# Kernel optimization log

Measured on AMD Instinct MI355X. Metric: run time of the kernel, lower is better.

Reference implementation:

```python
import jax, jax.numpy as jnp
import numpy as np
import math

B, T, C, H, S = 2, 2048, 1024, 16, 16
HD = C // H
EPS = 1e-5


def setup_inputs() -> dict:
    key = jax.random.key(0)
    ks = jax.random.split(key, 20)
    sc = 1.0 / math.sqrt(C)
    inp = {
        "x": jax.random.normal(ks[0], (B, T, C), jnp.float32),
        # A_log_fwd: log(arange(1..S)) repeated over dim (as in __init__)
        "A_log": jnp.log(jnp.tile(jnp.arange(1, S + 1, dtype=jnp.float32), (C, 1))),
        # Linear weights stored (in, out); apply as x @ W + b
        "Wd": jax.random.normal(ks[1], (C, C), jnp.float32) * sc,
        "bd": jnp.full((C,), -3.0, jnp.float32),
        "WB": jax.random.normal(ks[2], (C, S), jnp.float32) * sc,
        "WC": jax.random.normal(ks[3], (C, S), jnp.float32) * sc,
        "Wq": jax.random.normal(ks[4], (C, C), jnp.float32) * sc,
        "bq": jnp.zeros((C,), jnp.float32),
        "Wk": jax.random.normal(ks[5], (C, C), jnp.float32) * sc,
        "bk": jnp.zeros((C,), jnp.float32),
        "Wv": jax.random.normal(ks[6], (C, C), jnp.float32) * sc,
        "bv": jnp.zeros((C,), jnp.float32),
        "Wx": jax.random.normal(ks[7], (C, C), jnp.float32) * sc,
        "bx": jnp.zeros((C,), jnp.float32),
        "Wo": jax.random.normal(ks[8], (C, C), jnp.float32) * sc,
        "bo": jnp.zeros((C,), jnp.float32),
        "ln_g": jnp.ones((C,), jnp.float32),
        "ln_b": jnp.zeros((C,), jnp.float32),
        "temp": jnp.full((1, H, 1, 1), 0.5, jnp.float32),
    }
    return inp


def _forward(x, A_log, Wd, bd, WB, WC, Wq, bq, Wk, bk, Wv, bv, Wx, bx, Wo, bo, ln_g, ln_b, temp):
    x_base = x @ Wx + bx                      # (B,T,C)
    delta = jax.nn.softplus(x @ Wd + bd)      # (B,T,C)
    B_mat = x @ WB                            # (B,T,S)
    C_mat = x @ WC                            # (B,T,S)
    A = -jnp.exp(A_log)                       # (C,S)

    def scan_fn(h, inp):
        xb_t, d_t, B_t, C_t = inp             # (B,C),(B,C),(B,S),(B,S)
        bar_A = jnp.exp(d_t[..., None] * A)   # (B,C,S)
        h = bar_A * h + (d_t * xb_t)[..., None] * B_t[:, None, :]
        y = jnp.einsum('bcs,bs->bc', h, C_t)
        return h, y

    h0 = jnp.zeros((B, C, S), x.dtype)
    xs = (jnp.swapaxes(x_base, 0, 1), jnp.swapaxes(delta, 0, 1),
          jnp.swapaxes(B_mat, 0, 1), jnp.swapaxes(C_mat, 0, 1))
    _, ys = jax.lax.scan(scan_fn, h0, xs)
    out_fwd = jnp.swapaxes(ys, 0, 1)          # (B,T,C)

    # LayerNorm(x_base + out_fwd)
    hyb = x_base + out_fwd
    mu = hyb.mean(-1, keepdims=True)
    var = hyb.var(-1, keepdims=True)
    hybrid = (hyb - mu) * jax.lax.rsqrt(var + EPS) * ln_g + ln_b

    def heads(W, b):
        return (hybrid @ W + b).reshape(B, T, H, HD).transpose(0, 2, 1, 3)

    Q, K, V = heads(Wq, bq), heads(Wk, bk), heads(Wv, bv)
    scores = jnp.einsum('bhqd,bhkd->bhqk', Q, K) / math.sqrt(HD)
    scores = scores * jax.nn.softplus(temp)
    mask = jnp.tril(jnp.ones((T, T), bool))
    scores = jnp.where(mask[None, None], scores, -jnp.inf)
    attn = jax.nn.softmax(scores, axis=-1)
    out = jnp.einsum('bhqk,bhkd->bhqd', attn, V).transpose(0, 2, 1, 3).reshape(B, T, C)
    return out @ Wo + bo


def reference(x, A_log, Wd, bd, WB, WC, Wq, bq, Wk, bk, Wv, bv, Wx, bx, Wo, bo, ln_g, ln_b, temp):
    return _forward(x, A_log, Wd, bd, WB, WC, Wq, bq, Wk, bk, Wv, bv, Wx, bx, Wo, bo, ln_g, ln_b, temp)
```

## Files before the change

kernel.cpp:

```cpp
#include <hip/hip_runtime.h>
#include <math.h>

#define B_  2
#define T_  2048
#define C_  1024
#define H_  16
#define S_  16
#define HD_ 64
#define NCH 32
#define CHL 64

typedef short  short8  __attribute__((ext_vector_type(8)));
typedef unsigned short ushort8 __attribute__((ext_vector_type(8)));
typedef unsigned short ushort4v __attribute__((ext_vector_type(4)));
typedef float  f32x4   __attribute__((ext_vector_type(4)));

__device__ __forceinline__ float softplus_f(float v) {
    return fmaxf(v, 0.f) + log1pf(__expf(-fabsf(v)));
}

__device__ __forceinline__ unsigned short f2bf(float x) {
    unsigned u = __float_as_uint(x);
    u += 0x7fffu + ((u >> 16) & 1u);
    return (unsigned short)(u >> 16);
}

__device__ __forceinline__ void gload16(const unsigned short* g,
                                        unsigned short* l)
{
    __builtin_amdgcn_global_load_lds(
        (const __attribute__((address_space(1))) unsigned int*)g,
        (__attribute__((address_space(3))) unsigned int*)l, 16, 0, 0);
}

__global__ __launch_bounds__(256) void cast_bf16(const float* __restrict__ in,
                                                 unsigned short* __restrict__ out,
                                                 int n4)
{
    int i = blockIdx.x * 256 + threadIdx.x;
    if (i >= n4) return;
    float4 v = ((const float4*)in)[i];
    ushort4v o = {f2bf(v.x), f2bf(v.y), f2bf(v.z), f2bf(v.w)};
    ((ushort4v*)out)[i] = o;
}

__device__ __forceinline__ void wtrans_body(const float* __restrict__ W,
                                            unsigned short* __restrict__ WT,
                                            int bx, int by, int tid)
{
    __shared__ float t[32][33];
    const int n0 = bx * 32, k0 = by * 32;
    const int tx = tid & 31, ty = tid >> 5;
#pragma unroll
    for (int p = 0; p < 4; ++p)
        t[ty + p * 8][tx] = W[(size_t)(k0 + ty + p * 8) * C_ + n0 + tx];
    __syncthreads();
#pragma unroll
    for (int p = 0; p < 4; ++p)
        WT[(size_t)(n0 + ty + p * 8) * C_ + k0 + tx] = f2bf(t[tx][ty + p * 8]);
}

__global__ __launch_bounds__(256) void wtrans(const float* __restrict__ W,
                                              unsigned short* __restrict__ WT)
{
    wtrans_body(W, WT, blockIdx.x, blockIdx.y, threadIdx.x);
}

__global__ __launch_bounds__(256) void wtrans_multi(
    const float* __restrict__ Wx, const float* __restrict__ Wd,
    const float* __restrict__ Wq, const float* __restrict__ Wk,
    const float* __restrict__ Wv,
    unsigned short* __restrict__ Astack, unsigned short* __restrict__ Wqkv)
{
    const float* src;
    unsigned short* dst;
    switch (blockIdx.z) {
        case 0: src = Wx; dst = Astack; break;
        case 1: src = Wd; dst = Astack + (size_t)1024 * 1024; break;
        case 2: src = Wq; dst = Wqkv; break;
        case 3: src = Wk; dst = Wqkv + (size_t)1024 * 1024; break;
        default: src = Wv; dst = Wqkv + (size_t)2048 * 1024; break;
    }
    wtrans_body(src, dst, blockIdx.x, blockIdx.y, threadIdx.x);
}

__global__ __launch_bounds__(256) void prep_misc(
    const float* __restrict__ WB, const float* __restrict__ WC,
    const float* __restrict__ bx, const float* __restrict__ bd,
    const float* __restrict__ bq, const float* __restrict__ bk,
    const float* __restrict__ bv,
    unsigned short* __restrict__ Astack, float* __restrict__ biasPD,
    float* __restrict__ biasQKV)
{
    int gid = blockIdx.x * 256 + threadIdx.x;
    if (gid < 32768) {
        int w = gid >> 14, rem = gid & 16383;
        int s = rem >> 10, k = rem & 1023;
        const float* src = w ? WC : WB;
        Astack[(size_t)(2048 + w * 16 + s) * 1024 + k] = f2bf(src[k * 16 + s]);
    } else {
        int id = gid - 32768;
        if (id < 2176) {
            biasPD[id] = id < 1024 ? bx[id] : (id < 2048 ? bd[id - 1024] : 0.f);
        } else {
            int id2 = id - 2176;
            if (id2 < 3072)
                biasQKV[id2] = id2 < 1024 ? bq[id2]
                             : (id2 < 2048 ? bk[id2 - 1024] : bv[id2 - 2048]);
        }
    }
}

__global__ __launch_bounds__(256) void gemm_mfma(
    const unsigned short* __restrict__ A, const unsigned short* __restrict__ Bm,
    const float* __restrict__ bias,
    void* __restrict__ outv, void* __restrict__ out2,
    void* __restrict__ out3, void* __restrict__ out4,
    int M, int N, int K, int lda, int mode)
{
    __shared__ __align__(16) unsigned short As[4][4096];
    __shared__ __align__(16) unsigned short Bs[4][4096];

    const int tid = threadIdx.x;
    const int w = tid >> 6, lane = tid & 63;
    const int lq = lane & 15, lg = lane >> 4;
    const int wm = w >> 1, wn = w & 1;
    const int mBase = blockIdx.y * 128, nBase = blockIdx.x * 128;

    A  += (size_t)blockIdx.z * K;
    Bm += (size_t)blockIdx.z * K;

    const int c0 = tid, c1 = tid + 256;
    const int rA0 = ((c0 >> 6) << 4) + (c0 & 15), kO0 = ((c0 >> 4) & 3) << 3;
    const int rA1 = ((c1 >> 6) << 4) + (c1 & 15), kO1 = ((c1 >> 4) & 3) << 3;

    const int wL0 = w * 512;
    const int wL1 = 2048 + w * 512;

    f32x4 acc[4][4];
#pragma unroll
    for (int i = 0; i < 4; ++i)
#pragma unroll
        for (int j = 0; j < 4; ++j) acc[i][j] = (f32x4){0.f, 0.f, 0.f, 0.f};

    const unsigned short* ga0 = A  + (size_t)(mBase + rA0) * lda + kO0;
    const unsigned short* ga1 = A  + (size_t)(mBase + rA1) * lda + kO1;
    const unsigned short* gb0 = Bm + (size_t)(nBase + rA0) * lda + kO0;
    const unsigned short* gb1 = Bm + (size_t)(nBase + rA1) * lda + kO1;

    #define STAGE(bufv, k0v)                               \
        do {                                               \
            gload16(ga0 + (k0v), &As[bufv][wL0]);          \
            gload16(ga1 + (k0v), &As[bufv][wL1]);          \
            gload16(gb0 + (k0v), &Bs[bufv][wL0]);          \
            gload16(gb1 + (k0v), &Bs[bufv][wL1]);          \
        } while (0)
    #define COMPUTE(bufv)                                                       \
        do {                                                                    \
            short8 a[4], b[4];                                                  \
            _Pragma("unroll")                                                   \
            for (int i = 0; i < 4; ++i)                                         \
                a[i] = *(const short8*)&As[bufv][((wm * 4 + i) * 64 + lg * 16 + lq) * 8]; \
            _Pragma("unroll")                                                   \
            for (int j = 0; j < 4; ++j)                                         \
                b[j] = *(const short8*)&Bs[bufv][((wn * 4 + j) * 64 + lg * 16 + lq) * 8]; \
            _Pragma("unroll")                                                   \
            for (int i = 0; i < 4; ++i)                                         \
                _Pragma("unroll")                                               \
                for (int j = 0; j < 4; ++j)                                     \
                    acc[i][j] = __builtin_amdgcn_mfma_f32_16x16x32_bf16(        \
                        a[i], b[j], acc[i][j], 0, 0, 0);                        \
        } while (0)
    #define WAITV4() asm volatile("s_waitcnt vmcnt(4)" ::: "memory")
    #define WAITV0() asm volatile("s_waitcnt vmcnt(0)" ::: "memory")
    #define LGKM0()  asm volatile("s_waitcnt lgkmcnt(0)" ::: "memory")
    #define STEP(cbuf, kt)                                          \
        do {                                                        \
            if ((kt) + 32 < K) WAITV4(); else WAITV0();             \
            LGKM0();                                                \
            __builtin_amdgcn_s_barrier();                           \
            if ((kt) + 64 < K) STAGE(((cbuf) + 2) & 3, (kt) + 64);  \
            COMPUTE(cbuf);                                          \
        } while (0)

    STAGE(0, 0);
    STAGE(1, 32);

    for (int k0 = 0; k0 < K; k0 += 128) {
        STEP(0, k0);
        STEP(1, k0 + 32);
        STEP(2, k0 + 64);
        STEP(3, k0 + 96);
    }
    #undef STAGE
    #undef COMPUTE
    #undef WAITV4
    #undef WAITV0
    #undef LGKM0
    #undef STEP

    if (mode == 0) {
        float* O = blockIdx.z ? (float*)out2 : (float*)outv;
#pragma unroll
        for (int i = 0; i < 4; ++i) {
            int Rb = mBase + wm * 64 + i * 16 + lg * 4;
#pragma unroll
            for (int j = 0; j < 4; ++j) {
                int Cg = nBase + wn * 64 + j * 16 + lq;
#pragma unroll
                for (int r = 0; r < 4; ++r)
                    O[(size_t)(Rb + r) * N + Cg] = acc[i][j][r];
            }
        }
    } else if (mode == 1) {
        float* xbaseT = (float*)outv;
        float* deltaT = (float*)out2;
        float* BmT    = (float*)out3;
        float* CmT    = (float*)out4;
#pragma unroll
        for (int i = 0; i < 4; ++i) {
            int Rb = mBase + wm * 64 + i * 16 + lg * 4;
            if (Rb >= 2080) continue;
            float bb[4];
#pragma unroll
            for (int r = 0; r < 4; ++r) bb[r] = bias[Rb + r];
#pragma unroll
            for (int j = 0; j < 4; ++j) {
                int Cg = nBase + wn * 64 + j * 16 + lq;
                int b = Cg >> 11, t = Cg & (T_ - 1);
#pragma unroll
                for (int r = 0; r < 4; ++r) {
                    int R = Rb + r;
                    float v = acc[i][j][r] + bb[r];
                    if (Rb < 1024) {
                        xbaseT[((size_t)b * C_ + R) * T_ + t] = v;
                    } else if (Rb < 2048) {
                        deltaT[((size_t)b * C_ + (R - 1024)) * T_ + t] =
                            softplus_f(v);
                    } else if (Rb < 2064) {
                        BmT[((size_t)b * S_ + (R - 2048)) * T_ + t] = v;
                    } else {
                        CmT[((size_t)b * S_ + (R - 2064)) * T_ + t] = v;
                    }
                }
            }
        }
    } else {
        unsigned short* Qb  = (unsigned short*)outv;
        unsigned short* Kb  = (unsigned short*)out2;
        unsigned short* VTb = (unsigned short*)out3;
#pragma unroll
        for (int j = 0; j < 4; ++j) {
            int Cg = nBase + wn * 64 + j * 16 + lq;
            int reg = Cg >> 10, c = Cg & 1023;
            int h = c >> 6, hd = c & 63;
            float bb = bias[Cg];
#pragma unroll
            for (int i = 0; i < 4; ++i) {
                int Rb = mBase + wm * 64 + i * 16 + lg * 4;
#pragma unroll
                for (int r = 0; r < 4; ++r) {
                    int R = Rb + r, b = R >> 11, t = R & (T_ - 1);
                    unsigned short o = f2bf(acc[i][j][r] + bb);
                    if (reg == 0)
                        Qb[(((size_t)(b * H_ + h) * T_ + t) * HD_) + hd] = o;
                    else if (reg == 1)
                        Kb[(((size_t)(b * H_ + h) * T_ + t) * HD_) + hd] = o;
                    else
                        VTb[(((size_t)(b * H_ + h) * HD_ + hd) * T_) + t] = o;
                }
            }
        }
    }
}

__global__ __launch_bounds__(256) void combine_out(
    const float* __restrict__ p0, const float* __restrict__ p1,
    const float* __restrict__ bo, float* __restrict__ out)
{
    int i = blockIdx.x * 256 + threadIdx.x;
    float4 a = ((const float4*)p0)[i];
    float4 b = ((const float4*)p1)[i];
    float4 bb = ((const float4*)bo)[i & 255];
    float4 o = {a.x + b.x + bb.x, a.y + b.y + bb.y,
                a.z + b.z + bb.z, a.w + b.w + bb.w};
    ((float4*)out)[i] = o;
}

__global__ __launch_bounds__(256) void scan_partial(
    const float* __restrict__ xbaseT, const float* __restrict__ deltaT,
    const float* __restrict__ BmT, const float* __restrict__ A_log,
    float4* __restrict__ Pbuf, float4* __restrict__ Lbuf)
{
    const int tid = threadIdx.x;
    const int s4 = tid & 3;
    const int cm = tid >> 2;
    const int cg = blockIdx.x & 15;
    const int k  = (blockIdx.x >> 4) & (NCH - 1);
    const int b  = blockIdx.x >> 9;
    const int c  = cg * 64 + cm;

    float a[4];
#pragma unroll
    for (int j = 0; j < 4; ++j)
        a[j] = -__expf(A_log[c * S_ + s4 * 4 + j]);

    const int tb = k * CHL;
    const float* dp = deltaT + ((size_t)b * C_ + c) * T_ + tb;
    const float* xp = xbaseT + ((size_t)b * C_ + c) * T_ + tb;
    const float* bp = BmT + ((size_t)(b * S_ + s4 * 4)) * T_ + tb;

    float L[4] = {0.f, 0.f, 0.f, 0.f};
    float sumd = 0.f;
    for (int t0 = 0; t0 < CHL; t0 += 4) {
        float4 d4 = *(const float4*)&dp[t0];
        float4 x4 = *(const float4*)&xp[t0];
        float dv[4] = {d4.x, d4.y, d4.z, d4.w};
        float xv[4] = {x4.x, x4.y, x4.z, x4.w};
        float bv[4][4];
#pragma unroll
        for (int j = 0; j < 4; ++j) {
            float4 b4 = *(const float4*)&bp[(size_t)j * T_ + t0];
            bv[j][0] = b4.x; bv[j][1] = b4.y; bv[j][2] = b4.z; bv[j][3] = b4.w;
        }
#pragma unroll
        for (int q = 0; q < 4; ++q) {
            float u = dv[q] * xv[q];
            sumd += dv[q];
#pragma unroll
            for (int j = 0; j < 4; ++j)
                L[j] = fmaf(__expf(dv[q] * a[j]), L[j], u * bv[j][q]);
        }
    }
    int gid = blockIdx.x * 256 + tid;
    float4 P4 = {__expf(a[0] * sumd), __expf(a[1] * sumd),
                 __expf(a[2] * sumd), __expf(a[3] * sumd)};
    float4 L4 = {L[0], L[1], L[2], L[3]};
    Pbuf[gid] = P4;
    Lbuf[gid] = L4;
}

__global__ __launch_bounds__(256) void scan_final(
    const float* __restrict__ xbaseT, const float* __restrict__ deltaT,
    const float* __restrict__ BmT, const float* __restrict__ CmT,
    const float* __restrict__ A_log, const float4* __restrict__ Pbuf,
    const float4* __restrict__ Lbuf, float* __restrict__ hyb)
{
    const int tid = threadIdx.x;
    const int s4 = tid & 3;
    const int cm = tid >> 2;
    const int cg = blockIdx.x & 15;
    const int k  = (blockIdx.x >> 4) & (NCH - 1);
    const int b  = blockIdx.x >> 9;
    const int c  = cg * 64 + cm;

    float h[4] = {0.f, 0.f, 0.f, 0.f};
    for (int k2 = 0; k2 < k; ++k2) {
        int gid2 = (((b * NCH + k2) << 4) + cg) * 256 + tid;
        float4 P4 = Pbuf[gid2];
        float4 L4 = Lbuf[gid2];
        h[0] = fmaf(P4.x, h[0], L4.x);
        h[1] = fmaf(P4.y, h[1], L4.y);
        h[2] = fmaf(P4.z, h[2], L4.z);
        h[3] = fmaf(P4.w, h[3], L4.w);
    }

    float a[4];
#pragma unroll
    for (int j = 0; j < 4; ++j)
        a[j] = -__expf(A_log[c * S_ + s4 * 4 + j]);

    const int tb = k * CHL;
    const float* dp = deltaT + ((size_t)b * C_ + c) * T_ + tb;
    const float* xp = xbaseT + ((size_t)b * C_ + c) * T_ + tb;
    const float* bp = BmT + ((size_t)(b * S_ + s4 * 4)) * T_ + tb;
    const float* cp = CmT + ((size_t)(b * S_ + s4 * 4)) * T_ + tb;
    float* hp = hyb + ((size_t)b * T_ + tb) * C_ + c;

    for (int t0 = 0; t0 < CHL; t0 += 4) {
        float4 d4 = *(const float4*)&dp[t0];
        float4 x4 = *(const float4*)&xp[t0];
        float dv[4] = {d4.x, d4.y, d4.z, d4.w};
        float xv[4] = {x4.x, x4.y, x4.z, x4.w};
        float bv[4][4], cv[4][4];
#pragma unroll
        for (int j = 0; j < 4; ++j) {
            float4 b4 = *(const float4*)&bp[(size_t)j * T_ + t0];
            float4 c4 = *(const float4*)&cp[(size_t)j * T_ + t0];
            bv[j][0] = b4.x; bv[j][1] = b4.y; bv[j][2] = b4.z; bv[j][3] = b4.w;
            cv[j][0] = c4.x; cv[j][1] = c4.y; cv[j][2] = c4.z; cv[j][3] = c4.w;
        }
#pragma unroll
        for (int q = 0; q < 4; ++q) {
            float u = dv[q] * xv[q];
#pragma unroll
            for (int j = 0; j < 4; ++j)
                h[j] = fmaf(__expf(dv[q] * a[j]), h[j], u * bv[j][q]);
            float y = h[0] * cv[0][q];
            y = fmaf(h[1], cv[1][q], y);
            y = fmaf(h[2], cv[2][q], y);
            y = fmaf(h[3], cv[3][q], y);
            y += __shfl_xor(y, 1, 64);
            y += __shfl_xor(y, 2, 64);
            if (s4 == 0) hp[(size_t)(t0 + q) * C_] = xv[q] + y;
        }
    }
}

__global__ __launch_bounds__(256) void layernorm_kernel(
    const float* __restrict__ in, const float* __restrict__ g,
    const float* __restrict__ beta, unsigned short* __restrict__ out)
{
    const int row = blockIdx.x;
    const float* rp = in + (size_t)row * C_;
    const int c = threadIdx.x * 4;
    float4 v = *(const float4*)&rp[c];
    float sum = v.x + v.y + v.z + v.w;
    float sq = v.x * v.x + v.y * v.y + v.z * v.z + v.w * v.w;
#pragma unroll
    for (int off = 1; off < 64; off <<= 1) {
        sum += __shfl_xor(sum, off, 64);
        sq += __shfl_xor(sq, off, 64);
    }
    __shared__ float sS[4], sQ[4];
    int wave = threadIdx.x >> 6, lane = threadIdx.x & 63;
    if (lane == 0) { sS[wave] = sum; sQ[wave] = sq; }
    __syncthreads();
    sum = sS[0] + sS[1] + sS[2] + sS[3];
    sq = sQ[0] + sQ[1] + sQ[2] + sQ[3];
    const float mu = sum * (1.f / C_);
    const float var = sq * (1.f / C_) - mu * mu;
    const float rstd = rsqrtf(var + 1e-5f);
    float4 gg = *(const float4*)&g[c];
    float4 bb = *(const float4*)&beta[c];
    ushort4v o;
    o.x = f2bf((v.x - mu) * rstd * gg.x + bb.x);
    o.y = f2bf((v.y - mu) * rstd * gg.y + bb.y);
    o.z = f2bf((v.z - mu) * rstd * gg.z + bb.z);
    o.w = f2bf((v.w - mu) * rstd * gg.w + bb.w);
    *(ushort4v*)&out[(size_t)row * C_ + c] = o;
}

#define BKT 128
#define KP  72
#define VP  136
__global__ __launch_bounds__(256) void attn_mfma(
    const unsigned short* __restrict__ Q, const unsigned short* __restrict__ K,
    const unsigned short* __restrict__ VT, const float* __restrict__ temp,
    unsigned short* __restrict__ out)
{
    __shared__ __align__(16) unsigned short Ks[BKT * KP];
    __shared__ __align__(16) unsigned short Vs[80 * VP];
    __shared__ __align__(16) unsigned short Ps[64 * VP];

    const int tid = threadIdx.x;
    const int w = tid >> 6, lane = tid & 63;
    const int lq = lane & 15, lg = lane >> 4;
    const int p  = blockIdx.x & 15;
    const int bh = blockIdx.x >> 4;
    const int b = bh >> 4, h = bh & 15;

    const float scale = softplus_f(temp[h]) * 0.125f;
    const unsigned short* Qp = Q + (size_t)bh * T_ * HD_;
    const unsigned short* Kp = K + (size_t)bh * T_ * HD_;
    const unsigned short* Vp = VT + (size_t)bh * HD_ * T_;

    {
        int r = 64 + (tid >> 4), o = (tid & 15) * 8;
        ushort8 ones = {0x3f80, 0x3f80, 0x3f80, 0x3f80,
                        0x3f80, 0x3f80, 0x3f80, 0x3f80};
        *(ushort8*)&Vs[r * VP + o] = ones;
    }

    ushort8 kreg[4], vreg[4];
    #define LOADKV(jtv)                                                        \
        do {                                                                   \
            int kb = (jtv) * BKT;                                              \
            _Pragma("unroll")                                                  \
            for (int q2 = 0; q2 < 4; ++q2) {                                   \
                int c = tid + q2 * 256;                                        \
                kreg[q2] = *(const ushort8*)&Kp[(size_t)(kb + (c >> 3)) * HD_  \
                                                + (c & 7) * 8];                \
                vreg[q2] = *(const ushort8*)&Vp[(size_t)(c >> 4) * T_ + kb     \
                                                + (c & 15) * 8];               \
            }                                                                  \
        } while (0)

    for (int half = 0; half < 2; ++half) {
        const int qi = half ? p : (31 - p);
        const int qbase = qi * 64;
        const int nT = (qbase + 64 + BKT - 1) / BKT;

        short8 qf[2];
#pragma unroll
        for (int s = 0; s < 2; ++s)
            qf[s] = *(const short8*)&Qp[(size_t)(qbase + w * 16 + lq) * HD_
                                        + s * 32 + lg * 8];
        LOADKV(0);

        float m_i[4];
        f32x4 o[5];
#pragma unroll
        for (int r = 0; r < 4; ++r) m_i[r] = -INFINITY;
#pragma unroll
        for (int j = 0; j < 5; ++j) o[j] = (f32x4){0.f, 0.f, 0.f, 0.f};

        for (int jt = 0; jt < nT; ++jt) {
            const int kbase = jt * BKT;
            const bool last = (jt == nT - 1);
            __syncthreads();
#pragma unroll
            for (int q2 = 0; q2 < 4; ++q2) {
                int c = tid + q2 * 256;
                *(ushort8*)&Ks[(c >> 3) * KP + (c & 7) * 8] = kreg[q2];
                *(ushort8*)&Vs[(c >> 4) * VP + (c & 15) * 8] = vreg[q2];
            }
            __syncthreads();
            if (jt + 1 < nT) LOADKV(jt + 1);

            f32x4 sacc[8];
#pragma unroll
            for (int j = 0; j < 8; ++j) sacc[j] = (f32x4){0.f, 0.f, 0.f, 0.f};
#pragma unroll
            for (int s = 0; s < 2; ++s) {
#pragma unroll
                for (int j = 0; j < 8; ++j) {
                    short8 kf = *(const short8*)&Ks[(j * 16 + lq) * KP
                                                    + s * 32 + lg * 8];
                    sacc[j] = __builtin_amdgcn_mfma_f32_16x16x32_bf16(
                        qf[s], kf, sacc[j], 0, 0, 0);
                }
            }

#pragma unroll
            for (int r = 0; r < 4; ++r) {
                int qrow = qbase + w * 16 + lg * 4 + r;
                float sv[8];
#pragma unroll
                for (int j = 0; j < 8; ++j) {
                    sv[j] = sacc[j][r] * scale;
                    if (last && (kbase + j * 16 + lq > qrow)) sv[j] = -INFINITY;
                }
                float mx = sv[0];
#pragma unroll
                for (int j = 1; j < 8; ++j) mx = fmaxf(mx, sv[j]);
                mx = fmaxf(mx, __shfl_xor(mx, 1, 64));
                mx = fmaxf(mx, __shfl_xor(mx, 2, 64));
                mx = fmaxf(mx, __shfl_xor(mx, 4, 64));
                mx = fmaxf(mx, __shfl_xor(mx, 8, 64));
                float mnew = fmaxf(m_i[r], mx);
                float alpha = __expf(m_i[r] - mnew);
                m_i[r] = mnew;
#pragma unroll
                for (int j = 0; j < 5; ++j) o[j][r] *= alpha;
#pragma unroll
                for (int j = 0; j < 8; ++j)
                    Ps[(w * 16 + lg * 4 + r) * VP + j * 16 + lq] =
                        f2bf(__expf(sv[j] - mnew));
            }

#pragma unroll
            for (int s2 = 0; s2 < 4; ++s2) {
                short8 pf = *(const short8*)&Ps[(w * 16 + lq) * VP
                                                + s2 * 32 + lg * 8];
#pragma unroll
                for (int j = 0; j < 5; ++j) {
                    short8 vf = *(const short8*)&Vs[(j * 16 + lq) * VP
                                                    + s2 * 32 + lg * 8];
                    o[j] = __builtin_amdgcn_mfma_f32_16x16x32_bf16(
                        pf, vf, o[j], 0, 0, 0);
                }
            }
        }

#pragma unroll
        for (int r = 0; r < 4; ++r) {
            float inv = 1.f / o[4][r];
            int qrow = qbase + w * 16 + lg * 4 + r;
#pragma unroll
            for (int j = 0; j < 4; ++j)
                out[((size_t)(b * T_ + qrow)) * C_ + h * 64 + j * 16 + lq] =
                    f2bf(o[j][r] * inv);
        }
    }
    #undef LOADKV
}

extern "C" void kernel_launch(void* const* d_in, const int* in_sizes, int n_in,
                              void* d_out, int out_size, void* d_ws, size_t ws_size,
                              hipStream_t stream)
{
    const float* x     = (const float*)d_in[0];
    const float* A_log = (const float*)d_in[1];
    const float* Wd    = (const float*)d_in[2];
    const float* bd    = (const float*)d_in[3];
    const float* WB    = (const float*)d_in[4];
    const float* WC    = (const float*)d_in[5];
    const float* Wq    = (const float*)d_in[6];
    const float* bq    = (const float*)d_in[7];
    const float* Wk    = (const float*)d_in[8];
    const float* bk    = (const float*)d_in[9];
    const float* Wv    = (const float*)d_in[10];
    const float* bv    = (const float*)d_in[11];
    const float* Wx    = (const float*)d_in[12];
    const float* bx    = (const float*)d_in[13];
    const float* Wo    = (const float*)d_in[14];
    const float* bo    = (const float*)d_in[15];
    const float* ln_g  = (const float*)d_in[16];
    const float* ln_b  = (const float*)d_in[17];
    const float* temp  = (const float*)d_in[18];

    char* wsb = (char*)d_ws;
    const size_t MB = 1024 * 1024;
    const size_t HMB = 512 * 1024;
    unsigned short* xb      = (unsigned short*)(wsb);
    float4* Pbuf            = (float4*)(wsb);
    float4* Lbuf            = (float4*)(wsb + 4 * MB);
    unsigned short* hybrid  = (unsigned short*)(wsb);
    float* P1               = (float*)(wsb);
    unsigned short* Astack  = (unsigned short*)(wsb + 8 * MB);
    float* biasPD           = (float*)(wsb + 8 * MB + (size_t)2176 * 2048);
    float* biasQKV          = biasPD + 2176;
    unsigned short* WqkvT   = (unsigned short*)(wsb + 12 * MB + HMB);
    unsigned short* WoT     = (unsigned short*)(wsb + 18 * MB + HMB);
    float* deltaT           = (float*)(wsb + 18 * MB + HMB);
    float* xbaseT           = (float*)(wsb + 34 * MB + HMB);
    float* hyb              = (float*)(wsb + 50 * MB + HMB);
    float* BmT              = (float*)(wsb + 66 * MB + HMB);
    float* CmT              = BmT + (size_t)B_ * S_ * T_;
    unsigned short* Qb      = (unsigned short*)(wsb + 20 * MB + HMB);
    unsigned short* Kb      = (unsigned short*)(wsb + 28 * MB + HMB);
    unsigned short* VTb     = (unsigned short*)(wsb + 36 * MB + HMB);
    unsigned short* attnO   = (unsigned short*)(wsb + 44 * MB + HMB);
    float* P0               = (float*)(wsb + 20 * MB + HMB);

    cast_bf16<<<4096, 256, 0, stream>>>(x, xb, (B_ * T_ * C_) / 4);
    wtrans_multi<<<dim3(32, 32, 5), 256, 0, stream>>>(Wx, Wd, Wq, Wk, Wv,
                                                      Astack, WqkvT);
    prep_misc<<<149, 256, 0, stream>>>(WB, WC, bx, bd, bq, bk, bv,
                                       Astack, biasPD, biasQKV);

    gemm_mfma<<<dim3(32, 17, 1), 256, 0, stream>>>(
        Astack, xb, biasPD, xbaseT, deltaT, BmT, CmT,
        2176, 4096, 1024, 1024, 1);

    const int scanBlocks = B_ * NCH * (C_ / 64);
    scan_partial<<<scanBlocks, 256, 0, stream>>>(xbaseT, deltaT, BmT, A_log,
                                                 Pbuf, Lbuf);
    scan_final<<<scanBlocks, 256, 0, stream>>>(xbaseT, deltaT, BmT, CmT, A_log,
                                               Pbuf, Lbuf, hyb);

    layernorm_kernel<<<B_ * T_, 256, 0, stream>>>(hyb, ln_g, ln_b, hybrid);

    gemm_mfma<<<dim3(24, 32, 1), 256, 0, stream>>>(
        hybrid, WqkvT, biasQKV, Qb, Kb, VTb, nullptr,
        4096, 3072, 1024, 1024, 2);

    attn_mfma<<<B_ * H_ * 16, 256, 0, stream>>>(Qb, Kb, VTb, temp, attnO);

    wtrans<<<dim3(32, 32), 256, 0, stream>>>(Wo, WoT);
    gemm_mfma<<<dim3(8, 32, 2), 256, 0, stream>>>(
        attnO, WoT, nullptr, P0, P1, nullptr, nullptr,
        4096, 1024, 512, 1024, 0);
    combine_out<<<4096, 256, 0, stream>>>(P0, P1, bo, (float*)d_out);
}
```

Measured before the change: 474.0 us.

## Use 256x256-tile 512-thread MFMA GEMM for the input and QKV projections

Adds a new GEMM kernel with 256x256 output tiles, 8 waves and double-buffered 64-wide K stages in LDS, and uses it for the fused input projection and the QKV projection. The old 128-tile kernel is kept only for the output projection and is reduced to its plain-store epilogue. Larger tiles give more data reuse per LDS load and fewer global reads. In exchange the grids shrink to 144 and 192 blocks, fewer than the CUs on the device. The 128KB LDS footprint allows only one block per CU, and the 2176-row projection now reads A rows past the end of the matrix.

```diff
diff --git a/kernel.cpp b/kernel.cpp
--- a/kernel.cpp
+++ b/kernel.cpp
@@ -111,12 +111,154 @@
     }
 }
 
-__global__ __launch_bounds__(256) void gemm_mfma(
+__global__ __launch_bounds__(512, 2) void gemm_mfma(
     const unsigned short* __restrict__ A, const unsigned short* __restrict__ Bm,
     const float* __restrict__ bias,
     void* __restrict__ outv, void* __restrict__ out2,
     void* __restrict__ out3, void* __restrict__ out4,
     int M, int N, int K, int lda, int mode)
+{
+    __shared__ __align__(16) unsigned short As[2][16384];
+    __shared__ __align__(16) unsigned short Bs[2][16384];
+
+    const int tid = threadIdx.x;
+    const int w = tid >> 6, lane = tid & 63;
+    const int lq = lane & 15, lg = lane >> 4;
+    const int wm = w >> 2, wn = w & 3;
+    const int mBase = blockIdx.y * 256, nBase = blockIdx.x * 256;
+
+    const unsigned short* gA[4];
+    const unsigned short* gB[4];
+    int ldsOff[4];
+#pragma unroll
+    for (int q = 0; q < 4; ++q) {
+        int c = tid + q * 512;
+        int row = ((c >> 7) << 4) + (c & 15);
+        int kofs = ((c >> 4) & 7) << 3;
+        gA[q] = A  + (size_t)(mBase + row) * lda + kofs;
+        gB[q] = Bm + (size_t)(nBase + row) * lda + kofs;
+        ldsOff[q] = c * 8;
+    }
+
+    f32x4 acc[8][4];
+#pragma unroll
+    for (int i = 0; i < 8; ++i)
+#pragma unroll
+        for (int j = 0; j < 4; ++j) acc[i][j] = (f32x4){0.f, 0.f, 0.f, 0.f};
+
+    #define STAGE(bufv, kt)                                   \
+        do {                                                  \
+            _Pragma("unroll")                                 \
+            for (int q = 0; q < 4; ++q) {                     \
+                gload16(gA[q] + (kt), &As[bufv][ldsOff[q]]);  \
+                gload16(gB[q] + (kt), &Bs[bufv][ldsOff[q]]);  \
+            }                                                 \
+        } while (0)
+    #define COMPUTE(bufv)                                                        \
+        do {                                                                     \
+            _Pragma("unroll")                                                    \
+            for (int s = 0; s < 2; ++s) {                                        \
+                short8 a[8], b[4];                                               \
+                _Pragma("unroll")                                                \
+                for (int i = 0; i < 8; ++i)                                      \
+                    a[i] = *(const short8*)&As[bufv][(wm * 8 + i) * 1024         \
+                                                     + (s * 4 + lg) * 128        \
+                                                     + lq * 8];                  \
+                _Pragma("unroll")                                                \
+                for (int j = 0; j < 4; ++j)                                      \
+                    b[j] = *(const short8*)&Bs[bufv][(wn * 4 + j) * 1024         \
+                                                     + (s * 4 + lg) * 128        \
+                                                     + lq * 8];                  \
+                _Pragma("unroll")                                                \
+                for (int i = 0; i < 8; ++i)                                      \
+                    _Pragma("unroll")                                            \
+                    for (int j = 0; j < 4; ++j)                                  \
+                        acc[i][j] = __builtin_amdgcn_mfma_f32_16x16x32_bf16(     \
+                            a[i], b[j], acc[i][j], 0, 0, 0);                     \
+            }                                                                    \
+        } while (0)
+
+    STAGE(0, 0);
+    __syncthreads();
+    const int nt = K >> 6;
+    for (int t = 0; t < nt; t += 2) {
+        if (t + 1 < nt) STAGE(1, (t + 1) << 6);
+        COMPUTE(0);
+        __syncthreads();
+        if (t + 2 < nt) STAGE(0, (t + 2) << 6);
+        COMPUTE(1);
+        __syncthreads();
+    }
+    #undef STAGE
+    #undef COMPUTE
+
+    if (mode == 1) {
+        float* xbaseT = (float*)outv;
+        float* deltaT = (float*)out2;
+        float* BmT    = (float*)out3;
+        float* CmT    = (float*)out4;
+#pragma unroll
+        for (int i = 0; i < 8; ++i) {
+            int Rb = mBase + wm * 128 + i * 16 + lg * 4;
+            if (Rb >= 2080) continue;
+            float bb[4];
+#pragma unroll
+            for (int r = 0; r < 4; ++r) bb[r] = bias[Rb + r];
+#pragma unroll
+            for (int j = 0; j < 4; ++j) {
+                int Cg = nBase + wn * 64 + j * 16 + lq;
+                int b = Cg >> 11, t = Cg & (T_ - 1);
+#pragma unroll
+                for (int r = 0; r < 4; ++r) {
+                    int R = Rb + r;
+                    float v = acc[i][j][r] + bb[r];
+                    if (Rb < 1024) {
+                        xbaseT[((size_t)b * C_ + R) * T_ + t] = v;
+                    } else if (Rb < 2048) {
+                        deltaT[((size_t)b * C_ + (R - 1024)) * T_ + t] =
+                            softplus_f(v);
+                    } else if (Rb < 2064) {
+                        BmT[((size_t)b * S_ + (R - 2048)) * T_ + t] = v;
+                    } else {
+                        CmT[((size_t)b * S_ + (R - 2064)) * T_ + t] = v;
+                    }
+                }
+            }
+        }
+    } else {
+        unsigned short* Qb  = (unsigned short*)outv;
+        unsigned short* Kb  = (unsigned short*)out2;
+        unsigned short* VTb = (unsigned short*)out3;
+#pragma unroll
+        for (int j = 0; j < 4; ++j) {
+            int Cg = nBase + wn * 64 + j * 16 + lq;
+            int reg = Cg >> 10, c = Cg & 1023;
+            int h = c >> 6, hd = c & 63;
+            float bb = bias[Cg];
+#pragma unroll
+            for (int i = 0; i < 8; ++i) {
+                int Rb = mBase + wm * 128 + i * 16 + lg * 4;
+#pragma unroll
+                for (int r = 0; r < 4; ++r) {
+                    int R = Rb + r, b = R >> 11, t = R & (T_ - 1);
+                    unsigned short o = f2bf(acc[i][j][r] + bb);
+                    if (reg == 0)
+                        Qb[(((size_t)(b * H_ + h) * T_ + t) * HD_) + hd] = o;
+                    else if (reg == 1)
+                        Kb[(((size_t)(b * H_ + h) * T_ + t) * HD_) + hd] = o;
+                    else
+                        VTb[(((size_t)(b * H_ + h) * HD_ + hd) * T_) + t] = o;
+                }
+            }
+        }
+    }
+}
+
+__global__ __launch_bounds__(256) void gemm_mfma128(
+    const unsigned short* __restrict__ A, const unsigned short* __restrict__ Bm,
+    const float* __restrict__ bias,
+    void* __restrict__ outv, void* __restrict__ out2,
+    int M, int N, int K, int lda)
 {
     __shared__ __align__(16) unsigned short As[4][4096];
     __shared__ __align__(16) unsigned short Bs[4][4096];
@@ -199,77 +341,16 @@
     #undef LGKM0
     #undef STEP
 
-    if (mode == 0) {
-        float* O = blockIdx.z ? (float*)out2 : (float*)outv;
-#pragma unroll
-        for (int i = 0; i < 4; ++i) {
-            int Rb = mBase + wm * 64 + i * 16 + lg * 4;
-#pragma unroll
-            for (int j = 0; j < 4; ++j) {
-                int Cg = nBase + wn * 64 + j * 16 + lq;
-#pragma unroll
-                for (int r = 0; r < 4; ++r)
-                    O[(size_t)(Rb + r) * N + Cg] = acc[i][j][r];
-            }
-        }
-    } else if (mode == 1) {
-        float* xbaseT = (float*)outv;
-        float* deltaT = (float*)out2;
-        float* BmT    = (float*)out3;
-        float* CmT    = (float*)out4;
-#pragma unroll
-        for (int i = 0; i < 4; ++i) {
-            int Rb = mBase + wm * 64 + i * 16 + lg * 4;
-            if (Rb >= 2080) continue;
-            float bb[4];
-#pragma unroll
-            for (int r = 0; r < 4; ++r) bb[r] = bias[Rb + r];
-#pragma unroll
-            for (int j = 0; j < 4; ++j) {
-                int Cg = nBase + wn * 64 + j * 16 + lq;
-                int b = Cg >> 11, t = Cg & (T_ - 1);
-#pragma unroll
-                for (int r = 0; r < 4; ++r) {
-                    int R = Rb + r;
-                    float v = acc[i][j][r] + bb[r];
-                    if (Rb < 1024) {
-                        xbaseT[((size_t)b * C_ + R) * T_ + t] = v;
-                    } else if (Rb < 2048) {
-                        deltaT[((size_t)b * C_ + (R - 1024)) * T_ + t] =
-                            softplus_f(v);
-                    } else if (Rb < 2064) {
-                        BmT[((size_t)b * S_ + (R - 2048)) * T_ + t] = v;
-                    } else {
-                        CmT[((size_t)b * S_ + (R - 2064)) * T_ + t] = v;
-                    }
-                }
-            }
-        }
-    } else {
-        unsigned short* Qb  = (unsigned short*)outv;
-        unsigned short* Kb  = (unsigned short*)out2;
-        unsigned short* VTb = (unsigned short*)out3;
+    float* O = blockIdx.z ? (float*)out2 : (float*)outv;
+#pragma unroll
+    for (int i = 0; i < 4; ++i) {
+        int Rb = mBase + wm * 64 + i * 16 + lg * 4;
 #pragma unroll
         for (int j = 0; j < 4; ++j) {
             int Cg = nBase + wn * 64 + j * 16 + lq;
-            int reg = Cg >> 10, c = Cg & 1023;
-            int h = c >> 6, hd = c & 63;
-            float bb = bias[Cg];
-#pragma unroll
-            for (int i = 0; i < 4; ++i) {
-                int Rb = mBase + wm * 64 + i * 16 + lg * 4;
-#pragma unroll
-                for (int r = 0; r < 4; ++r) {
-                    int R = Rb + r, b = R >> 11, t = R & (T_ - 1);
-                    unsigned short o = f2bf(acc[i][j][r] + bb);
-                    if (reg == 0)
-                        Qb[(((size_t)(b * H_ + h) * T_ + t) * HD_) + hd] = o;
-                    else if (reg == 1)
-                        Kb[(((size_t)(b * H_ + h) * T_ + t) * HD_) + hd] = o;
-                    else
-                        VTb[(((size_t)(b * H_ + h) * HD_ + hd) * T_) + t] = o;
-                }
-            }
+#pragma unroll
+            for (int r = 0; r < 4; ++r)
+                O[(size_t)(Rb + r) * N + Cg] = acc[i][j][r];
         }
     }
 }
@@ -640,7 +721,7 @@
     prep_misc<<<149, 256, 0, stream>>>(WB, WC, bx, bd, bq, bk, bv,
                                        Astack, biasPD, biasQKV);
 
-    gemm_mfma<<<dim3(32, 17, 1), 256, 0, stream>>>(
+    gemm_mfma<<<dim3(16, 9, 1), 512, 0, stream>>>(
         Astack, xb, biasPD, xbaseT, deltaT, BmT, CmT,
         2176, 4096, 1024, 1024, 1);
 
@@ -652,15 +733,15 @@
 
     layernorm_kernel<<<B_ * T_, 256, 0, stream>>>(hyb, ln_g, ln_b, hybrid);
 
-    gemm_mfma<<<dim3(24, 32, 1), 256, 0, stream>>>(
+    gemm_mfma<<<dim3(12, 16, 1), 512, 0, stream>>>(
         hybrid, WqkvT, biasQKV, Qb, Kb, VTb, nullptr,
         4096, 3072, 1024, 1024, 2);
 
     attn_mfma<<<B_ * H_ * 16, 256, 0, stream>>>(Qb, Kb, VTb, temp, attnO);
 
     wtrans<<<dim3(32, 32), 256, 0, stream>>>(Wo, WoT);
-    gemm_mfma<<<dim3(8, 32, 2), 256, 0, stream>>>(
-        attnO, WoT, nullptr, P0, P1, nullptr, nullptr,
-        4096, 1024, 512, 1024, 0);
+    gemm_mfma128<<<dim3(8, 32, 2), 256, 0, stream>>>(
+        attnO, WoT, nullptr, P0, P1,
+        4096, 1024, 512, 1024);
     combine_out<<<4096, 256, 0, stream>>>(P0, P1, bo, (float*)d_out);
 }
```

Measured after the change: 527.8 us. 11.3% more time.

## Add 256x256-tile 512-thread MFMA GEMM for input and QKV projections

Applied to the files above, without the earlier changes.

Introduces a new GEMM kernel that uses 256x256 output tiles with 8 waves, double-buffered LDS split into K halves, and interleaved global prefetch with barrier-gated phases and s_setprio around the MFMA bursts. The input projection and QKV projection launch this kernel, while the output projection keeps the 128x128 kernel, now specialised to the plain store mode. Larger tiles raise arithmetic intensity and cut global loads per FLOP. In exchange the grids become small (144 and 192 blocks) relative to the CU count, and register pressure rises to 32 accumulators per lane. The M=2176 input-projection GEMM is padded to 2304 rows, which wastes some work.

```diff
diff --git a/kernel.cpp b/kernel.cpp
--- a/kernel.cpp
+++ b/kernel.cpp
@@ -111,12 +111,175 @@
     }
 }
 
-__global__ __launch_bounds__(256) void gemm_mfma(
+__global__ __launch_bounds__(512, 2) void gemm_mfma256(
     const unsigned short* __restrict__ A, const unsigned short* __restrict__ Bm,
     const float* __restrict__ bias,
     void* __restrict__ outv, void* __restrict__ out2,
     void* __restrict__ out3, void* __restrict__ out4,
     int M, int N, int K, int lda, int mode)
+{
+    __shared__ __align__(16) unsigned short AS[2][2][8192];
+    __shared__ __align__(16) unsigned short BS[2][2][8192];
+
+    const int tid = threadIdx.x;
+    const int w = tid >> 6, lane = tid & 63;
+    const int lq = lane & 15, lg = lane >> 4;
+    const int wm = w >> 2, wn = w & 3;
+    const int mBase = blockIdx.y * 256, nBase = blockIdx.x * 256;
+
+    const int c0 = tid, c1 = tid + 512;
+    const int r0 = ((c0 >> 6) << 4) | (c0 & 15), k0l = ((c0 >> 4) & 3) << 3;
+    const int r1 = ((c1 >> 6) << 4) | (c1 & 15), k1l = ((c1 >> 4) & 3) << 3;
+    const unsigned short* gA0 = A  + (size_t)(mBase + r0) * lda + k0l;
+    const unsigned short* gA1 = A  + (size_t)(mBase + r1) * lda + k1l;
+    const unsigned short* gB0 = Bm + (size_t)(nBase + r0) * lda + k0l;
+    const unsigned short* gB1 = Bm + (size_t)(nBase + r1) * lda + k1l;
+
+    f32x4 acc[8][4];
+#pragma unroll
+    for (int i = 0; i < 8; ++i)
+#pragma unroll
+        for (int j = 0; j < 4; ++j) acc[i][j] = (f32x4){0.f, 0.f, 0.f, 0.f};
+
+    #define STG_A(buf_, half_, kb_)                                           \
+        do {                                                                  \
+            gload16(gA0 + (kb_) + (half_) * 32, &AS[buf_][half_][c0 * 8]);    \
+            gload16(gA1 + (kb_) + (half_) * 32, &AS[buf_][half_][c1 * 8]);    \
+        } while (0)
+    #define STG_B(buf_, half_, kb_)                                           \
+        do {                                                                  \
+            gload16(gB0 + (kb_) + (half_) * 32, &BS[buf_][half_][c0 * 8]);    \
+            gload16(gB1 + (kb_) + (half_) * 32, &BS[buf_][half_][c1 * 8]);    \
+        } while (0)
+    #define WAITV8() asm volatile("s_waitcnt vmcnt(8)" ::: "memory")
+    #define WAITV4() asm volatile("s_waitcnt vmcnt(4)" ::: "memory")
+    #define WAITV0() asm volatile("s_waitcnt vmcnt(0)" ::: "memory")
+
+    #define PHASE(buf_, half_, qi_, STAGE_STMT, GATE_STMT)                    \
+        do {                                                                  \
+            short8 a_[4];                                                     \
+            _Pragma("unroll")                                                 \
+            for (int i = 0; i < 4; ++i)                                       \
+                a_[i] = *(const short8*)&AS[buf_][half_]                      \
+                    [((wm * 8 + (qi_) * 4 + i) * 64 + lg * 16 + lq) * 8];     \
+            if ((qi_) == 0) {                                                 \
+                _Pragma("unroll")                                             \
+                for (int j = 0; j < 4; ++j)                                   \
+                    bfr[j] = *(const short8*)&BS[buf_][half_]                 \
+                        [((wn * 4 + j) * 64 + lg * 16 + lq) * 8];             \
+            }                                                                 \
+            STAGE_STMT;                                                       \
+            __builtin_amdgcn_s_barrier();                                     \
+            asm volatile("s_waitcnt lgkmcnt(0)" ::: "memory");                \
+            __builtin_amdgcn_s_setprio(1);                                    \
+            _Pragma("unroll")                                                 \
+            for (int i = 0; i < 4; ++i)                                       \
+                _Pragma("unroll")                                             \
+                for (int j = 0; j < 4; ++j)                                   \
+                    acc[(qi_) * 4 + i][j] =                                   \
+                        __builtin_amdgcn_mfma_f32_16x16x32_bf16(              \
+                            a_[i], bfr[j], acc[(qi_) * 4 + i][j], 0, 0, 0);   \
+            __builtin_amdgcn_s_setprio(0);                                    \
+            GATE_STMT;                                                        \
+            __builtin_amdgcn_s_barrier();                                     \
+        } while (0)
+
+    STG_A(0, 0, 0);
+    STG_B(0, 0, 0);
+    STG_A(0, 1, 0);
+    STG_B(0, 1, 0);
+    STG_A(1, 0, 64);
+    STG_B(1, 0, 64);
+    WAITV8();
+    __builtin_amdgcn_s_barrier();
+
+    const int NT = K >> 6;
+    for (int kt = 0; kt < NT; ++kt) {
+        const int buf = kt & 1, nbuf = buf ^ 1;
+        const int kb1 = (kt + 1) << 6, kb2 = (kt + 2) << 6;
+        short8 bfr[4];
+        PHASE(buf, 0, 0, { if (kt + 1 < NT) STG_A(nbuf, 1, kb1); }, {});
+        PHASE(buf, 0, 1, { if (kt + 1 < NT) STG_B(nbuf, 1, kb1); },
+              { if (kt < NT - 1) WAITV8(); else WAITV0(); });
+        PHASE(buf, 1, 0, { if (kt + 2 < NT) STG_A(buf, 0, kb2); }, {});
+        PHASE(buf, 1, 1, { if (kt + 2 < NT) STG_B(buf, 0, kb2); },
+              { if (kt < NT - 2) WAITV8();
+                else if (kt == NT - 2) WAITV4(); });
+    }
+    #undef STG_A
+    #undef STG_B
+    #undef WAITV8
+    #undef WAITV4
+    #undef WAITV0
+    #undef PHASE
+
+    if (mode == 1) {
+        float* xbaseT = (float*)outv;
+        float* deltaT = (float*)out2;
+        float* BmT    = (float*)out3;
+        float* CmT    = (float*)out4;
+#pragma unroll
+        for (int i = 0; i < 8; ++i) {
+            int Rb = mBase + wm * 128 + i * 16 + lg * 4;
+            if (Rb >= 2080) continue;
+            float bb[4];
+#pragma unroll
+            for (int r = 0; r < 4; ++r) bb[r] = bias[Rb + r];
+#pragma unroll
+            for (int j = 0; j < 4; ++j) {
+                int Cg = nBase + wn * 64 + j * 16 + lq;
+                int b = Cg >> 11, t = Cg & (T_ - 1);
+#pragma unroll
+                for (int r = 0; r < 4; ++r) {
+                    int R = Rb + r;
+                    float v = acc[i][j][r] + bb[r];
+                    if (Rb < 1024) {
+                        xbaseT[((size_t)b * C_ + R) * T_ + t] = v;
+                    } else if (Rb < 2048) {
+                        deltaT[((size_t)b * C_ + (R - 1024)) * T_ + t] =
+                            softplus_f(v);
+                    } else if (Rb < 2064) {
+                        BmT[((size_t)b * S_ + (R - 2048)) * T_ + t] = v;
+                    } else {
+                        CmT[((size_t)b * S_ + (R - 2064)) * T_ + t] = v;
+                    }
+                }
+            }
+        }
+    } else {
+        unsigned short* Qb  = (unsigned short*)outv;
+        unsigned short* Kb  = (unsigned short*)out2;
+        unsigned short* VTb = (unsigned short*)out3;
+#pragma unroll
+        for (int j = 0; j < 4; ++j) {
+            int Cg = nBase + wn * 64 + j * 16 + lq;
+            int reg = Cg >> 10, c = Cg & 1023;
+            int h = c >> 6, hd = c & 63;
+            float bb = bias[Cg];
+#pragma unroll
+            for (int i = 0; i < 8; ++i) {
+                int Rb = mBase + wm * 128 + i * 16 + lg * 4;
+#pragma unroll
+                for (int r = 0; r < 4; ++r) {
+                    int R = Rb + r, b = R >> 11, t = R & (T_ - 1);
+                    unsigned short o = f2bf(acc[i][j][r] + bb);
+                    if (reg == 0)
+                        Qb[(((size_t)(b * H_ + h) * T_ + t) * HD_) + hd] = o;
+                    else if (reg == 1)
+                        Kb[(((size_t)(b * H_ + h) * T_ + t) * HD_) + hd] = o;
+                    else
+                        VTb[(((size_t)(b * H_ + h) * HD_ + hd) * T_) + t] = o;
+                }
+            }
+        }
+    }
+}
+
+__global__ __launch_bounds__(256) void gemm_mfma128(
+    const unsigned short* __restrict__ A, const unsigned short* __restrict__ Bm,
+    const float* __restrict__ bias,
+    void* __restrict__ outv, void* __restrict__ out2,
+    int M, int N, int K, int lda)
 {
     __shared__ __align__(16) unsigned short As[4][4096];
     __shared__ __align__(16) unsigned short Bs[4][4096];
@@ -199,77 +362,16 @@
     #undef LGKM0
     #undef STEP
 
-    if (mode == 0) {
-        float* O = blockIdx.z ? (float*)out2 : (float*)outv;
-#pragma unroll
-        for (int i = 0; i < 4; ++i) {
-            int Rb = mBase + wm * 64 + i * 16 + lg * 4;
-#pragma unroll
-            for (int j = 0; j < 4; ++j) {
-                int Cg = nBase + wn * 64 + j * 16 + lq;
-#pragma unroll
-                for (int r = 0; r < 4; ++r)
-                    O[(size_t)(Rb + r) * N + Cg] = acc[i][j][r];
-            }
-        }
-    } else if (mode == 1) {
-        float* xbaseT = (float*)outv;
-        float* deltaT = (float*)out2;
-        float* BmT    = (float*)out3;
-        float* CmT    = (float*)out4;
-#pragma unroll
-        for (int i = 0; i < 4; ++i) {
-            int Rb = mBase + wm * 64 + i * 16 + lg * 4;
-            if (Rb >= 2080) continue;
-            float bb[4];
-#pragma unroll
-            for (int r = 0; r < 4; ++r) bb[r] = bias[Rb + r];
-#pragma unroll
-            for (int j = 0; j < 4; ++j) {
-                int Cg = nBase + wn * 64 + j * 16 + lq;
-                int b = Cg >> 11, t = Cg & (T_ - 1);
-#pragma unroll
-                for (int r = 0; r < 4; ++r) {
-                    int R = Rb + r;
-                    float v = acc[i][j][r] + bb[r];
-                    if (Rb < 1024) {
-                        xbaseT[((size_t)b * C_ + R) * T_ + t] = v;
-                    } else if (Rb < 2048) {
-                        deltaT[((size_t)b * C_ + (R - 1024)) * T_ + t] =
-                            softplus_f(v);
-                    } else if (Rb < 2064) {
-                        BmT[((size_t)b * S_ + (R - 2048)) * T_ + t] = v;
-                    } else {
-                        CmT[((size_t)b * S_ + (R - 2064)) * T_ + t] = v;
-                    }
-                }
-            }
-        }
-    } else {
-        unsigned short* Qb  = (unsigned short*)outv;
-        unsigned short* Kb  = (unsigned short*)out2;
-        unsigned short* VTb = (unsigned short*)out3;
+    float* O = blockIdx.z ? (float*)out2 : (float*)outv;
+#pragma unroll
+    for (int i = 0; i < 4; ++i) {
+        int Rb = mBase + wm * 64 + i * 16 + lg * 4;
 #pragma unroll
         for (int j = 0; j < 4; ++j) {
             int Cg = nBase + wn * 64 + j * 16 + lq;
-            int reg = Cg >> 10, c = Cg & 1023;
-            int h = c >> 6, hd = c & 63;
-            float bb = bias[Cg];
-#pragma unroll
-            for (int i = 0; i < 4; ++i) {
-                int Rb = mBase + wm * 64 + i * 16 + lg * 4;
-#pragma unroll
-                for (int r = 0; r < 4; ++r) {
-                    int R = Rb + r, b = R >> 11, t = R & (T_ - 1);
-                    unsigned short o = f2bf(acc[i][j][r] + bb);
-                    if (reg == 0)
-                        Qb[(((size_t)(b * H_ + h) * T_ + t) * HD_) + hd] = o;
-                    else if (reg == 1)
-                        Kb[(((size_t)(b * H_ + h) * T_ + t) * HD_) + hd] = o;
-                    else
-                        VTb[(((size_t)(b * H_ + h) * HD_ + hd) * T_) + t] = o;
-                }
-            }
+#pragma unroll
+            for (int r = 0; r < 4; ++r)
+                O[(size_t)(Rb + r) * N + Cg] = acc[i][j][r];
         }
     }
 }
@@ -640,7 +742,7 @@
     prep_misc<<<149, 256, 0, stream>>>(WB, WC, bx, bd, bq, bk, bv,
                                        Astack, biasPD, biasQKV);
 
-    gemm_mfma<<<dim3(32, 17, 1), 256, 0, stream>>>(
+    gemm_mfma256<<<dim3(16, 9, 1), 512, 0, stream>>>(
         Astack, xb, biasPD, xbaseT, deltaT, BmT, CmT,
         2176, 4096, 1024, 1024, 1);
 
@@ -652,15 +754,15 @@
 
     layernorm_kernel<<<B_ * T_, 256, 0, stream>>>(hyb, ln_g, ln_b, hybrid);
 
-    gemm_mfma<<<dim3(24, 32, 1), 256, 0, stream>>>(
+    gemm_mfma256<<<dim3(12, 16, 1), 512, 0, stream>>>(
         hybrid, WqkvT, biasQKV, Qb, Kb, VTb, nullptr,
         4096, 3072, 1024, 1024, 2);
 
     attn_mfma<<<B_ * H_ * 16, 256, 0, stream>>>(Qb, Kb, VTb, temp, attnO);
 
     wtrans<<<dim3(32, 32), 256, 0, stream>>>(Wo, WoT);
-    gemm_mfma<<<dim3(8, 32, 2), 256, 0, stream>>>(
-        attnO, WoT, nullptr, P0, P1, nullptr, nullptr,
-        4096, 1024, 512, 1024, 0);
+    gemm_mfma128<<<dim3(8, 32, 2), 256, 0, stream>>>(
+        attnO, WoT, nullptr, P0, P1,
+        4096, 1024, 512, 1024);
     combine_out<<<4096, 256, 0, stream>>>(P0, P1, bo, (float*)d_out);
 }
```

New measurement: 489.8 us. 1.03x slower.
